# Kernel optimization log

Hardware: AMD Instinct MI355X
Metric: run time of the kernel (lower is better)

## Reference

```python
import math
import jax, jax.numpy as jnp
import numpy as np

B, S, IN_DIM = 8, 1024, 3
D, H, FF, L, OUT = 512, 8, 2048, 4, 6
DH = D // H


def layernorm(x, g, b, eps=1e-5):
    mu = jnp.mean(x, axis=-1, keepdims=True)
    var = jnp.mean((x - mu) ** 2, axis=-1, keepdims=True)
    return (x - mu) * jax.lax.rsqrt(var + eps) * g + b


def positional_encoding(seq_len, d):
    pos = jnp.arange(seq_len, dtype=jnp.float32)[:, None]
    div = jnp.exp(jnp.arange(0, d, 2, dtype=jnp.float32) * (-math.log(10000.0) / d))
    pe = jnp.zeros((seq_len, d), dtype=jnp.float32)
    pe = pe.at[:, 0::2].set(jnp.sin(pos * div))
    pe = pe.at[:, 1::2].set(jnp.cos(pos * div))
    return pe  # [S, D]


def setup_inputs() -> dict:
    key = jax.random.key(0)
    ks = jax.random.split(key, 16)
    s = 0.02
    inp = {
        'x': jax.random.normal(ks[0], (B, S, IN_DIM), dtype=jnp.float32),
        'Wproj': jax.random.normal(ks[1], (IN_DIM, D), dtype=jnp.float32) * s,
        'bproj': jnp.zeros((D,), jnp.float32),
        'gp': jnp.ones((D,), jnp.float32), 'bp': jnp.zeros((D,), jnp.float32),
        'Wq': jax.random.normal(ks[2], (L, D, D), dtype=jnp.float32) * s,
        'Wk': jax.random.normal(ks[3], (L, D, D), dtype=jnp.float32) * s,
        'Wv': jax.random.normal(ks[4], (L, D, D), dtype=jnp.float32) * s,
        'Wo': jax.random.normal(ks[5], (L, D, D), dtype=jnp.float32) * s,
        'g1': jnp.ones((L, D), jnp.float32), 'b1': jnp.zeros((L, D), jnp.float32),
        'W1': jax.random.normal(ks[6], (L, D, FF), dtype=jnp.float32) * s,
        'W2': jax.random.normal(ks[7], (L, FF, D), dtype=jnp.float32) * s,
        'g2': jnp.ones((L, D), jnp.float32), 'b2': jnp.zeros((L, D), jnp.float32),
        'gf': jnp.ones((D,), jnp.float32), 'bf': jnp.zeros((D,), jnp.float32),
        'Wout': jax.random.normal(ks[8], (D, OUT), dtype=jnp.float32) * s,
        'bout': jnp.zeros((OUT,), jnp.float32),
    }
    return inp


def reference(x, Wproj, bproj, gp, bp, Wq, Wk, Wv, Wo, g1, b1,
              W1, W2, g2, b2, gf, bf, Wout, bout):
    # padding mask: True where all features are zero
    mask = jnp.sum(jnp.abs(x), axis=-1) == 0  # [B, S]
    h = x @ Wproj + bproj                     # [B, S, D]
    h = h + positional_encoding(h.shape[1], D)[None]
    h = layernorm(h, gp, bp)
    scale = 1.0 / math.sqrt(DH)
    for l in range(L):
        q = (h @ Wq[l]).reshape(B, S, H, DH)
        k = (h @ Wk[l]).reshape(B, S, H, DH)
        v = (h @ Wv[l]).reshape(B, S, H, DH)
        scores = jnp.einsum('bqhd,bkhd->bhqk', q, k) * scale  # [B,H,S,S]
        scores = jnp.where(mask[:, None, None, :], -jnp.inf, scores)
        attn = jax.nn.softmax(scores, axis=-1)
        o = jnp.einsum('bhqk,bkhd->bqhd', attn, v).reshape(B, S, D) @ Wo[l]
        h = layernorm(h + o, g1[l], b1[l])
        ff = jax.nn.silu(h @ W1[l]) @ W2[l]
        h = layernorm(h + ff, g2[l], b2[l])
    h = layernorm(h, gf, bf)
    not_pad = (~mask).astype(h.dtype)                      # [B, S]
    pooled = jnp.sum(h * not_pad[..., None], axis=1) / (
        jnp.sum(not_pad, axis=1, keepdims=True) + 1e-8)    # [B, D]
    return pooled @ Wout + bout                            # [B, OUT]
```

## Files before the change

### kernel.cpp

```cpp
#include <hip/hip_runtime.h>
#include <math.h>
#include <stdint.h>

namespace {

constexpr int Bc = 8, Sc = 1024, Dc = 512, Hc = 8, FFc = 2048, Lc = 4, OUTc = 6;
constexpr int QS = 1536;

typedef __attribute__((ext_vector_type(8))) short  bf16x8;
typedef __attribute__((ext_vector_type(4))) float  f32x4;

__device__ __forceinline__ void ld4(float d[4], const float* s) {
    float4 t = *(const float4*)s;
    d[0] = t.x; d[1] = t.y; d[2] = t.z; d[3] = t.w;
}
__device__ __forceinline__ float bf2f(unsigned short u) {
    union { uint32_t i; float f; } c; c.i = ((uint32_t)u) << 16; return c.f;
}
__device__ __forceinline__ unsigned short f2bf(float f) {
    union { float f; uint32_t i; } c; c.f = f;
    uint32_t r = c.i + 0x7FFF + ((c.i >> 16) & 1);
    return (unsigned short)(r >> 16);
}

#define GLDS16(gp, lp) __builtin_amdgcn_global_load_lds(                      \
    (const __attribute__((address_space(1))) uint32_t*)(gp),                  \
    (__attribute__((address_space(3))) uint32_t*)(lp), 16, 0, 0)

__global__ __launch_bounds__(256) void castAll(
    const float* __restrict__ Wq, const float* __restrict__ Wk,
    const float* __restrict__ Wv, const float* __restrict__ Wo,
    const float* __restrict__ W1, const float* __restrict__ W2,
    unsigned short* __restrict__ qkvT, unsigned short* __restrict__ WoT,
    unsigned short* __restrict__ W1T, unsigned short* __restrict__ W2T)
{
    const int t = blockIdx.x;
    const float* in; unsigned short* out; int K, N, k0, n0;
    if (t < 1024) {
        const int mat = t >> 6, l = mat >> 2, w = mat & 3;
        K = 512; N = 512;
        k0 = ((t >> 3) & 7) << 6; n0 = (t & 7) << 6;
        const float* ws4[4] = {Wq, Wk, Wv, Wo};
        in = ws4[w] + (size_t)l * 512 * 512;
        out = (w < 3) ? qkvT + (size_t)l * QS * 512 + (size_t)w * 512 * 512
                      : WoT + (size_t)l * 512 * 512;
    } else if (t < 2048) {
        const int u = t - 1024, l = u >> 8;
        K = 512; N = 2048;
        k0 = ((u >> 5) & 7) << 6; n0 = (u & 31) << 6;
        in = W1 + (size_t)l * 512 * 2048;
        out = W1T + (size_t)l * 2048 * 512;
    } else {
        const int u = t - 2048, l = u >> 8;
        K = 2048; N = 512;
        k0 = ((u >> 3) & 31) << 6; n0 = (u & 7) << 6;
        in = W2 + (size_t)l * 2048 * 512;
        out = W2T + (size_t)l * 512 * 2048;
    }
    __shared__ float tbuf[64][65];
    const int c = threadIdx.x & 63, r4 = threadIdx.x >> 6;
    #pragma unroll
    for (int it = 0; it < 16; ++it) {
        const int r = (it << 2) + r4;
        tbuf[r][c] = in[(size_t)(k0 + r) * N + n0 + c];
    }
    __syncthreads();
    #pragma unroll
    for (int it = 0; it < 16; ++it) {
        const int r = (it << 2) + r4;
        out[(size_t)(n0 + r) * K + k0 + c] = f2bf(tbuf[c][r]);
    }
}

__global__ __launch_bounds__(256) void proj_pe_ln(
    const float* __restrict__ x, const float* __restrict__ Wproj,
    const float* __restrict__ bproj, const float* __restrict__ gp,
    const float* __restrict__ bp, float* __restrict__ h,
    unsigned short* __restrict__ hbf, float* __restrict__ notpad,
    float* __restrict__ maskadd)
{
    const int wave = threadIdx.x >> 6, lane = threadIdx.x & 63;
    const int tok = (blockIdx.x << 2) + wave;
    const int s = tok & (Sc - 1);
    const float x0 = x[tok * 3 + 0], x1 = x[tok * 3 + 1], x2 = x[tok * 3 + 2];
    if (lane == 0) {
        const bool pad = (fabsf(x0) + fabsf(x1) + fabsf(x2) == 0.0f);
        notpad[tok]  = pad ? 0.0f : 1.0f;
        maskadd[tok] = pad ? -1e30f : 0.0f;
    }
    const float c = -logf(10000.0f) / (float)Dc;
    float v[8];
    float sum = 0.f, sumsq = 0.f;
    #pragma unroll
    for (int g = 0; g < 2; ++g) {
        const int dbase = (g << 8) + (lane << 2);
        #pragma unroll
        for (int j = 0; j < 4; ++j) {
            const int d = dbase + j;
            float val = fmaf(x0, Wproj[d],
                        fmaf(x1, Wproj[Dc + d],
                        fmaf(x2, Wproj[2 * Dc + d], bproj[d])));
            const float arg = (float)s * expf((float)(d & ~1) * c);
            val += (d & 1) ? cosf(arg) : sinf(arg);
            v[(g << 2) + j] = val;
            sum += val; sumsq += val * val;
        }
    }
    #pragma unroll
    for (int m = 1; m < 64; m <<= 1) {
        sum   += __shfl_xor(sum, m, 64);
        sumsq += __shfl_xor(sumsq, m, 64);
    }
    const float mu = sum * (1.0f / Dc);
    const float var = sumsq * (1.0f / Dc) - mu * mu;
    const float rstd = rsqrtf(var + 1e-5f);
    #pragma unroll
    for (int g = 0; g < 2; ++g) {
        const int dbase = (g << 8) + (lane << 2);
        float gg[4], bb[4];
        ld4(gg, gp + dbase); ld4(bb, bp + dbase);
        float4 r;
        r.x = (v[(g<<2)+0] - mu) * rstd * gg[0] + bb[0];
        r.y = (v[(g<<2)+1] - mu) * rstd * gg[1] + bb[1];
        r.z = (v[(g<<2)+2] - mu) * rstd * gg[2] + bb[2];
        r.w = (v[(g<<2)+3] - mu) * rstd * gg[3] + bb[3];
        *(float4*)(h + (size_t)tok * Dc + dbase) = r;
        ushort4 rb;
        rb.x = f2bf(r.x); rb.y = f2bf(r.y); rb.z = f2bf(r.z); rb.w = f2bf(r.w);
        *(ushort4*)(hbf + (size_t)tok * Dc + dbase) = rb;
    }
}

__global__ __launch_bounds__(256) void add_ln(
    const float* __restrict__ hin, const unsigned short* __restrict__ delta,
    const float* __restrict__ g, const float* __restrict__ b,
    float* __restrict__ hout, unsigned short* __restrict__ hbf)
{
    const int wave = threadIdx.x >> 6, lane = threadIdx.x & 63;
    const int tok = (blockIdx.x << 2) + wave;
    const float* hp = hin + (size_t)tok * Dc;
    float v[8];
    float sum = 0.f, sumsq = 0.f;
    #pragma unroll
    for (int gI = 0; gI < 2; ++gI) {
        const int dbase = (gI << 8) + (lane << 2);
        float a[4];
        ld4(a, hp + dbase);
        if (delta) {
            ushort4 d4 = *(const ushort4*)(delta + (size_t)tok * Dc + dbase);
            a[0] += bf2f(d4.x); a[1] += bf2f(d4.y);
            a[2] += bf2f(d4.z); a[3] += bf2f(d4.w);
        }
        #pragma unroll
        for (int j = 0; j < 4; ++j) {
            v[(gI << 2) + j] = a[j];
            sum += a[j]; sumsq += a[j] * a[j];
        }
    }
    #pragma unroll
    for (int m = 1; m < 64; m <<= 1) {
        sum   += __shfl_xor(sum, m, 64);
        sumsq += __shfl_xor(sumsq, m, 64);
    }
    const float mu = sum * (1.0f / Dc);
    const float var = sumsq * (1.0f / Dc) - mu * mu;
    const float rstd = rsqrtf(var + 1e-5f);
    #pragma unroll
    for (int gI = 0; gI < 2; ++gI) {
        const int dbase = (gI << 8) + (lane << 2);
        float gg[4], bb[4];
        ld4(gg, g + dbase); ld4(bb, b + dbase);
        float4 r;
        r.x = (v[(gI<<2)+0] - mu) * rstd * gg[0] + bb[0];
        r.y = (v[(gI<<2)+1] - mu) * rstd * gg[1] + bb[1];
        r.z = (v[(gI<<2)+2] - mu) * rstd * gg[2] + bb[2];
        r.w = (v[(gI<<2)+3] - mu) * rstd * gg[3] + bb[3];
        *(float4*)(hout + (size_t)tok * Dc + dbase) = r;
        if (hbf) {
            ushort4 rb;
            rb.x = f2bf(r.x); rb.y = f2bf(r.y); rb.z = f2bf(r.z); rb.w = f2bf(r.w);
            *(ushort4*)(hbf + (size_t)tok * Dc + dbase) = rb;
        }
    }
}

template<int EPI, int NT>
__global__ __launch_bounds__(256) void gemm_bf16(
    const unsigned short* __restrict__ A, const unsigned short* __restrict__ Bt,
    void* __restrict__ Cv, void* __restrict__ Cv2, int M, int N, int K)
{
    constexpr int JN = NT / 32;
    constexpr int ABsz = 128 * 64 + NT * 64;
    constexpr int TRst = 136;
    constexpr int SMsz = (EPI == 3 && 128 * TRst > ABsz) ? 128 * TRst : ABsz;
    __shared__ unsigned short smem[SMsz];
    unsigned short* As = smem;
    unsigned short* Bs = smem + 128 * 64;
    const int tid = threadIdx.x;
    const int wave = tid >> 6, lane = tid & 63;
    const int m0 = blockIdx.y << 7;
    const int n0 = blockIdx.x * NT;
    const int wm = (wave >> 1) << 6;
    const int wn = (wave & 1) * (NT / 2);
    const int l15 = lane & 15;
    const int lg  = lane >> 4;
    const int grow  = lane >> 3;
    const int gcolk = ((lane & 7) ^ grow) << 3;

    f32x4 acc[4][JN] = {};

    for (int k0 = 0; k0 < K; k0 += 64) {
        __syncthreads();
        #pragma unroll
        for (int t = 0; t < 4; ++t) {
            const int rb = (t << 5) + (wave << 3);
            GLDS16(A + (size_t)(m0 + rb + grow) * K + k0 + gcolk, &As[rb * 64]);
        }
        #pragma unroll
        for (int t = 0; t < NT / 32; ++t) {
            const int rb = (t << 5) + (wave << 3);
            GLDS16(Bt + (size_t)(n0 + rb + grow) * K + k0 + gcolk, &Bs[rb * 64]);
        }
        __syncthreads();
        #pragma unroll
        for (int h = 0; h < 2; ++h) {
            const int sw = (((h << 2) + lg) ^ (l15 & 7)) << 3;
            bf16x8 af[4], bfr[JN];
            #pragma unroll
            for (int i = 0; i < 4; ++i)
                af[i] = *(const bf16x8*)&As[(wm + (i << 4) + l15) * 64 + sw];
            #pragma unroll
            for (int j = 0; j < JN; ++j)
                bfr[j] = *(const bf16x8*)&Bs[(wn + (j << 4) + l15) * 64 + sw];
            #pragma unroll
            for (int i = 0; i < 4; ++i)
                #pragma unroll
                for (int j = 0; j < JN; ++j)
                    acc[i][j] = __builtin_amdgcn_mfma_f32_16x16x32_bf16(
                        af[i], bfr[j], acc[i][j], 0, 0, 0);
        }
    }

    if constexpr (EPI == 3) {
        if (n0 >= 1024) {
            __syncthreads();
            unsigned short* Tr = smem;
            #pragma unroll
            for (int i = 0; i < 4; ++i)
                #pragma unroll
                for (int j = 0; j < JN; ++j)
                    #pragma unroll
                    for (int r = 0; r < 4; ++r)
                        Tr[(wn + (j << 4) + l15) * TRst + wm + (i << 4) + (lg << 2) + r]
                            = f2bf(acc[i][j][r]);
            __syncthreads();
            const int bb = m0 >> 10, s0 = m0 & 1023;
            #pragma unroll
            for (int it = 0; it < 8; ++it) {
                const int idx = (it << 8) + tid;
                const int ln = idx >> 4, lmc = (idx & 15) << 3;
                const int gcol = n0 - 1024 + ln;
                const int head = gcol >> 6, dh = gcol & 63;
                *(bf16x8*)((unsigned short*)Cv2 +
                    (size_t)((((bb << 3) + head) << 6) + dh) * 1024 + s0 + lmc) =
                    *(const bf16x8*)&Tr[ln * TRst + lmc];
            }
            return;
        }
    }

    const int crow0 = m0 + wm + (lg << 2);
    const int ccol0 = n0 + wn + l15;
    #pragma unroll
    for (int i = 0; i < 4; ++i)
        #pragma unroll
        for (int j = 0; j < JN; ++j)
            #pragma unroll
            for (int r = 0; r < 4; ++r) {
                const int row = crow0 + (i << 4) + r;
                const int col = ccol0 + (j << 4);
                float v = acc[i][j][r];
                if (EPI == 3) {
                    if (n0 < 512) v *= 0.125f;
                    ((unsigned short*)Cv)[(size_t)row * 1024 + col] = f2bf(v);
                } else {
                    if (EPI == 1) v = v / (1.0f + expf(-v));
                    ((unsigned short*)Cv)[(size_t)row * N + col] = f2bf(v);
                }
            }
}

__global__ __launch_bounds__(256, 2) void attn_mfma(
    const unsigned short* __restrict__ qk,
    const unsigned short* __restrict__ vT,
    const float* __restrict__ maskadd,
    unsigned short* __restrict__ o)
{
    constexpr int PST = 124;
    __shared__ unsigned short Ks[2][128][32];
    __shared__ unsigned short Vs[4][64][32];
    __shared__ unsigned short Ps[4][32][PST];
    __shared__ float Madd[128];
    const int tid = threadIdx.x;
    const int wave = tid >> 6, lane = tid & 63;
    const int b  = blockIdx.x & 7;
    const int hh = (blockIdx.x >> 3) & 7;
    const int qt = blockIdx.x >> 6;
    const int q0 = qt << 7;
    const int l15 = lane & 15, lg = lane >> 4;
    const int srow = lane >> 2;
    const int scol = (lane & 3) << 3;

    #pragma unroll
    for (int t = 0; t < 2; ++t)
        #pragma unroll
        for (int p = 0; p < 2; ++p)
            GLDS16(qk + (size_t)((b << 10) + q0 + (t << 6) + (wave << 4) + srow) * 1024
                      + (hh << 6) + (p << 5) + scol,
                   &Ks[p][(t << 6) + (wave << 4)][0]);
    __syncthreads();
    bf16x8 qf[2][2];
    #pragma unroll
    for (int s = 0; s < 2; ++s)
        #pragma unroll
        for (int p = 0; p < 2; ++p)
            qf[s][p] = *(const bf16x8*)&Ks[p][(s << 6) + (wave << 4) + l15][lg << 3];

    f32x4 oacc[2][4] = {};
    float l_part[2][4] = {};

    for (int kt = 0; kt < 8; ++kt) {
        const int k0 = kt << 7;
        __syncthreads();
        #pragma unroll
        for (int t = 0; t < 2; ++t)
            #pragma unroll
            for (int p = 0; p < 2; ++p)
                GLDS16(qk + (size_t)((b << 10) + k0 + (t << 6) + (wave << 4) + srow) * 1024
                          + 512 + (hh << 6) + (p << 5) + scol,
                       &Ks[p][(t << 6) + (wave << 4)][0]);
        #pragma unroll
        for (int kp = 0; kp < 4; ++kp)
            GLDS16(vT + (size_t)((((b << 3) + hh) << 6) + (wave << 4) + srow) * 1024
                      + k0 + (kp << 5) + scol,
                   &Vs[kp][wave << 4][0]);
        if (tid < 128) Madd[tid] = maskadd[(b << 10) + k0 + tid];
        __syncthreads();

        f32x4 sacc[2][8] = {};
        #pragma unroll
        for (int j = 0; j < 8; ++j) {
            const bf16x8 kf0 = *(const bf16x8*)&Ks[0][(j << 4) + l15][lg << 3];
            const bf16x8 kf1 = *(const bf16x8*)&Ks[1][(j << 4) + l15][lg << 3];
            #pragma unroll
            for (int s = 0; s < 2; ++s) {
                sacc[s][j] = __builtin_amdgcn_mfma_f32_16x16x32_bf16(qf[s][0], kf0, sacc[s][j], 0, 0, 0);
                sacc[s][j] = __builtin_amdgcn_mfma_f32_16x16x32_bf16(qf[s][1], kf1, sacc[s][j], 0, 0, 0);
            }
        }

        #pragma unroll
        for (int s = 0; s < 2; ++s)
            #pragma unroll
            for (int j = 0; j < 8; ++j) {
                const float ma = Madd[(j << 4) + l15];
                #pragma unroll
                for (int r = 0; r < 4; ++r) {
                    const float p = __expf(sacc[s][j][r] + ma);
                    l_part[s][r] += p;
                    Ps[wave][(s << 4) + (lg << 2) + r][(j << 4) + l15] = f2bf(p);
                }
            }
        __asm__ volatile("s_waitcnt lgkmcnt(0)" ::: "memory");

        #pragma unroll
        for (int kp = 0; kp < 4; ++kp) {
            bf16x8 vf[4];
            #pragma unroll
            for (int j = 0; j < 4; ++j)
                vf[j] = *(const bf16x8*)&Vs[kp][(j << 4) + l15][lg << 3];
            #pragma unroll
            for (int s = 0; s < 2; ++s) {
                const bf16x8 pa = *(const bf16x8*)&Ps[wave][(s << 4) + l15][(kp << 5) + (lg << 3)];
                #pragma unroll
                for (int j = 0; j < 4; ++j)
                    oacc[s][j] = __builtin_amdgcn_mfma_f32_16x16x32_bf16(pa, vf[j], oacc[s][j], 0, 0, 0);
            }
        }
    }

    #pragma unroll
    for (int s = 0; s < 2; ++s)
        #pragma unroll
        for (int r = 0; r < 4; ++r) {
            float l = l_part[s][r];
            #pragma unroll
            for (int m = 1; m < 16; m <<= 1) l += __shfl_xor(l, m, 64);
            l_part[s][r] = 1.0f / l;
        }
    #pragma unroll
    for (int s = 0; s < 2; ++s) {
        const int tokr = (b << 10) + q0 + (s << 6) + (wave << 4) + (lg << 2);
        #pragma unroll
        for (int j = 0; j < 4; ++j)
            #pragma unroll
            for (int r = 0; r < 4; ++r)
                o[(size_t)(tokr + r) * 512 + (hh << 6) + (j << 4) + l15] =
                    f2bf(oacc[s][j][r] * l_part[s][r]);
    }
}

__global__ __launch_bounds__(256) void pool_kernel(
    const float* __restrict__ h, const float* __restrict__ notpad,
    float* __restrict__ pooled, float* __restrict__ counts)
{
    const int b = blockIdx.y;
    const int s0 = blockIdx.x << 5;
    const int t = threadIdx.x;
    float a0 = 0.f, a1 = 0.f;
    for (int ss = 0; ss < 32; ++ss) {
        const float w = notpad[(b << 10) + s0 + ss];
        const float* hp = h + (size_t)((b << 10) + s0 + ss) * Dc;
        a0 = fmaf(w, hp[t], a0);
        a1 = fmaf(w, hp[t + 256], a1);
    }
    atomicAdd(&pooled[b * Dc + t], a0);
    atomicAdd(&pooled[b * Dc + t + 256], a1);
    if (t < 32) {
        float w = notpad[(b << 10) + s0 + t];
        #pragma unroll
        for (int m = 1; m < 32; m <<= 1) w += __shfl_xor(w, m, 64);
        if (t == 0) atomicAdd(&counts[b], w);
    }
}

__global__ void out_kernel(
    const float* __restrict__ pooled, const float* __restrict__ counts,
    const float* __restrict__ Wout, const float* __restrict__ bout,
    float* __restrict__ out)
{
    const int bo = blockIdx.x;
    const int b = bo / OUTc, oc = bo % OUTc;
    const int lane = threadIdx.x;
    float acc = 0.f;
    for (int d = lane; d < Dc; d += 64)
        acc = fmaf(pooled[b * Dc + d], Wout[(size_t)d * OUTc + oc], acc);
    #pragma unroll
    for (int m = 1; m < 64; m <<= 1) acc += __shfl_xor(acc, m, 64);
    if (lane == 0) out[b * OUTc + oc] = acc / (counts[b] + 1e-8f) + bout[oc];
}

}

extern "C" void kernel_launch(void* const* d_in, const int* in_sizes, int n_in,
                              void* d_out, int out_size, void* d_ws, size_t ws_size,
                              hipStream_t stream)
{
    (void)in_sizes; (void)n_in; (void)out_size; (void)ws_size;
    const float* x     = (const float*)d_in[0];
    const float* Wproj = (const float*)d_in[1];
    const float* bproj = (const float*)d_in[2];
    const float* gp    = (const float*)d_in[3];
    const float* bp    = (const float*)d_in[4];
    const float* Wq    = (const float*)d_in[5];
    const float* Wk    = (const float*)d_in[6];
    const float* Wv    = (const float*)d_in[7];
    const float* Wo    = (const float*)d_in[8];
    const float* g1    = (const float*)d_in[9];
    const float* b1    = (const float*)d_in[10];
    const float* W1    = (const float*)d_in[11];
    const float* W2    = (const float*)d_in[12];
    const float* g2    = (const float*)d_in[13];
    const float* b2    = (const float*)d_in[14];
    const float* gf    = (const float*)d_in[15];
    const float* bf    = (const float*)d_in[16];
    const float* Wout  = (const float*)d_in[17];
    const float* bout  = (const float*)d_in[18];
    float* out = (float*)d_out;

    const size_t MiB = 1u << 20;
    char* base = (char*)d_ws;
    float*          h       = (float*)(base);
    unsigned short* h_bf    = (unsigned short*)(base + 16 * MiB);
    unsigned short* qk_act  = (unsigned short*)(base + 24 * MiB);
    unsigned short* vT      = (unsigned short*)(base + 40 * MiB);
    unsigned short* ob_bf   = (unsigned short*)(base + 48 * MiB);
    unsigned short* bufB_bf = (unsigned short*)(base + 56 * MiB);
    unsigned short* ffa_bf  = (unsigned short*)(base + 24 * MiB);
    unsigned short* qkvT    = (unsigned short*)(base + 72 * MiB);
    unsigned short* WoT     = (unsigned short*)(base + 78 * MiB);
    unsigned short* W1T     = (unsigned short*)(base + 80 * MiB);
    unsigned short* W2T     = (unsigned short*)(base + 88 * MiB);
    float*          notpad  = (float*)(base + 96 * MiB);
    float*          maskadd = notpad + 8192;
    float*          pooled  = maskadd + 8192;
    float*          counts  = pooled + Bc * Dc;

    const int M = Bc * Sc;

    castAll<<<3072, 256, 0, stream>>>(Wq, Wk, Wv, Wo, W1, W2, qkvT, WoT, W1T, W2T);
    proj_pe_ln<<<M / 4, 256, 0, stream>>>(x, Wproj, bproj, gp, bp, h, h_bf, notpad, maskadd);

    for (int l = 0; l < Lc; ++l) {
        gemm_bf16<3, 128><<<dim3(QS / 128, M / 128), 256, 0, stream>>>(
            h_bf, qkvT + (size_t)l * QS * 512, qk_act, vT, M, QS, 512);
        attn_mfma<<<Bc * Hc * (Sc / 128), 256, 0, stream>>>(qk_act, vT, maskadd, ob_bf);
        gemm_bf16<2, 64><<<dim3(512 / 64, M / 128), 256, 0, stream>>>(
            ob_bf, WoT + (size_t)l * 512 * 512, bufB_bf, nullptr, M, 512, 512);
        add_ln<<<M / 4, 256, 0, stream>>>(h, bufB_bf, g1 + (size_t)l * Dc, b1 + (size_t)l * Dc, h, h_bf);
        gemm_bf16<1, 128><<<dim3(FFc / 128, M / 128), 256, 0, stream>>>(
            h_bf, W1T + (size_t)l * FFc * 512, ffa_bf, nullptr, M, FFc, 512);
        gemm_bf16<2, 64><<<dim3(512 / 64, M / 128), 256, 0, stream>>>(
            ffa_bf, W2T + (size_t)l * 512 * FFc, bufB_bf, nullptr, M, 512, FFc);
        add_ln<<<M / 4, 256, 0, stream>>>(h, bufB_bf, g2 + (size_t)l * Dc, b2 + (size_t)l * Dc, h, h_bf);
    }
    add_ln<<<M / 4, 256, 0, stream>>>(h, nullptr, gf, bf, h, nullptr);

    hipMemsetAsync(pooled, 0, (size_t)(Bc * Dc + Bc) * sizeof(float), stream);
    pool_kernel<<<dim3(Sc / 32, Bc), 256, 0, stream>>>(h, notpad, pooled, counts);
    out_kernel<<<Bc * OUTc, 64, 0, stream>>>(pooled, counts, Wout, bout, out);
}
```

Before: 816.2 us.

## Keep residual in bf16, fuse final LN into pooling, coalesce GEMM epilogue

Removes the fp32 residual buffer so layernorm kernels read and write only bf16, halving residual traffic. The final layernorm is fused into the pooling kernel, and GEMM epilogues stage results through shared memory for vectorized coalesced stores. The attention kernel folds log2(e) into the Q scale to use exp2, uses cheaper bf16 rounding, and restructures P staging to halve shared memory. These changes trade residual precision for bandwidth and reduce kernel count.

```diff
diff --git a/kernel.cpp b/kernel.cpp
--- a/kernel.cpp
+++ b/kernel.cpp
@@ -16,11 +16,18 @@
 }
 __device__ __forceinline__ float bf2f(unsigned short u) {
     union { uint32_t i; float f; } c; c.i = ((uint32_t)u) << 16; return c.f;
+}
+__device__ __forceinline__ float bf2f_s(short u) {
+    union { uint32_t i; float f; } c; c.i = ((uint32_t)(unsigned short)u) << 16; return c.f;
 }
 __device__ __forceinline__ unsigned short f2bf(float f) {
     union { float f; uint32_t i; } c; c.f = f;
     uint32_t r = c.i + 0x7FFF + ((c.i >> 16) & 1);
     return (unsigned short)(r >> 16);
+}
+__device__ __forceinline__ unsigned short f2bf_fast(float f) {
+    union { float f; uint32_t i; } c; c.f = f;
+    return (unsigned short)((c.i + 0x8000u) >> 16);
 }
 
 #define GLDS16(gp, lp) __builtin_amdgcn_global_load_lds(                      \
@@ -75,9 +82,8 @@
 __global__ __launch_bounds__(256) void proj_pe_ln(
     const float* __restrict__ x, const float* __restrict__ Wproj,
     const float* __restrict__ bproj, const float* __restrict__ gp,
-    const float* __restrict__ bp, float* __restrict__ h,
-    unsigned short* __restrict__ hbf, float* __restrict__ notpad,
-    float* __restrict__ maskadd)
+    const float* __restrict__ bp, unsigned short* __restrict__ hbf,
+    float* __restrict__ notpad, float* __restrict__ maskadd)
 {
     const int wave = threadIdx.x >> 6, lane = threadIdx.x & 63;
     const int tok = (blockIdx.x << 2) + wave;
@@ -91,20 +97,17 @@
     const float c = -logf(10000.0f) / (float)Dc;
     float v[8];
     float sum = 0.f, sumsq = 0.f;
-    #pragma unroll
-    for (int g = 0; g < 2; ++g) {
-        const int dbase = (g << 8) + (lane << 2);
-        #pragma unroll
-        for (int j = 0; j < 4; ++j) {
-            const int d = dbase + j;
-            float val = fmaf(x0, Wproj[d],
-                        fmaf(x1, Wproj[Dc + d],
-                        fmaf(x2, Wproj[2 * Dc + d], bproj[d])));
-            const float arg = (float)s * expf((float)(d & ~1) * c);
-            val += (d & 1) ? cosf(arg) : sinf(arg);
-            v[(g << 2) + j] = val;
-            sum += val; sumsq += val * val;
-        }
+    const int d0 = lane << 3;
+    #pragma unroll
+    for (int j = 0; j < 8; ++j) {
+        const int d = d0 + j;
+        float val = fmaf(x0, Wproj[d],
+                    fmaf(x1, Wproj[Dc + d],
+                    fmaf(x2, Wproj[2 * Dc + d], bproj[d])));
+        const float arg = (float)s * expf((float)(d & ~1) * c);
+        val += (d & 1) ? cosf(arg) : sinf(arg);
+        v[j] = val;
+        sum += val; sumsq += val * val;
     }
     #pragma unroll
     for (int m = 1; m < 64; m <<= 1) {
@@ -112,50 +115,34 @@
         sumsq += __shfl_xor(sumsq, m, 64);
     }
     const float mu = sum * (1.0f / Dc);
-    const float var = sumsq * (1.0f / Dc) - mu * mu;
-    const float rstd = rsqrtf(var + 1e-5f);
-    #pragma unroll
-    for (int g = 0; g < 2; ++g) {
-        const int dbase = (g << 8) + (lane << 2);
-        float gg[4], bb[4];
-        ld4(gg, gp + dbase); ld4(bb, bp + dbase);
-        float4 r;
-        r.x = (v[(g<<2)+0] - mu) * rstd * gg[0] + bb[0];
-        r.y = (v[(g<<2)+1] - mu) * rstd * gg[1] + bb[1];
-        r.z = (v[(g<<2)+2] - mu) * rstd * gg[2] + bb[2];
-        r.w = (v[(g<<2)+3] - mu) * rstd * gg[3] + bb[3];
-        *(float4*)(h + (size_t)tok * Dc + dbase) = r;
-        ushort4 rb;
-        rb.x = f2bf(r.x); rb.y = f2bf(r.y); rb.z = f2bf(r.z); rb.w = f2bf(r.w);
-        *(ushort4*)(hbf + (size_t)tok * Dc + dbase) = rb;
-    }
+    const float rstd = rsqrtf(sumsq * (1.0f / Dc) - mu * mu + 1e-5f);
+    float gg[8], bb[8];
+    ld4(gg, gp + d0); ld4(gg + 4, gp + d0 + 4);
+    ld4(bb, bp + d0); ld4(bb + 4, bp + d0 + 4);
+    bf16x8 rb;
+    #pragma unroll
+    for (int j = 0; j < 8; ++j)
+        rb[j] = (short)f2bf((v[j] - mu) * rstd * gg[j] + bb[j]);
+    *(bf16x8*)(hbf + (size_t)tok * Dc + d0) = rb;
 }
 
 __global__ __launch_bounds__(256) void add_ln(
-    const float* __restrict__ hin, const unsigned short* __restrict__ delta,
+    const unsigned short* __restrict__ hin, const unsigned short* __restrict__ delta,
     const float* __restrict__ g, const float* __restrict__ b,
-    float* __restrict__ hout, unsigned short* __restrict__ hbf)
+    unsigned short* __restrict__ hout)
 {
     const int wave = threadIdx.x >> 6, lane = threadIdx.x & 63;
     const int tok = (blockIdx.x << 2) + wave;
-    const float* hp = hin + (size_t)tok * Dc;
+    const int d0 = lane << 3;
+    const size_t base = (size_t)tok * Dc + d0;
+    const bf16x8 hv = *(const bf16x8*)(hin + base);
+    const bf16x8 dv = *(const bf16x8*)(delta + base);
     float v[8];
     float sum = 0.f, sumsq = 0.f;
     #pragma unroll
-    for (int gI = 0; gI < 2; ++gI) {
-        const int dbase = (gI << 8) + (lane << 2);
-        float a[4];
-        ld4(a, hp + dbase);
-        if (delta) {
-            ushort4 d4 = *(const ushort4*)(delta + (size_t)tok * Dc + dbase);
-            a[0] += bf2f(d4.x); a[1] += bf2f(d4.y);
-            a[2] += bf2f(d4.z); a[3] += bf2f(d4.w);
-        }
-        #pragma unroll
-        for (int j = 0; j < 4; ++j) {
-            v[(gI << 2) + j] = a[j];
-            sum += a[j]; sumsq += a[j] * a[j];
-        }
+    for (int j = 0; j < 8; ++j) {
+        v[j] = bf2f_s(hv[j]) + bf2f_s(dv[j]);
+        sum += v[j]; sumsq += v[j] * v[j];
     }
     #pragma unroll
     for (int m = 1; m < 64; m <<= 1) {
@@ -163,25 +150,15 @@
         sumsq += __shfl_xor(sumsq, m, 64);
     }
     const float mu = sum * (1.0f / Dc);
-    const float var = sumsq * (1.0f / Dc) - mu * mu;
-    const float rstd = rsqrtf(var + 1e-5f);
-    #pragma unroll
-    for (int gI = 0; gI < 2; ++gI) {
-        const int dbase = (gI << 8) + (lane << 2);
-        float gg[4], bb[4];
-        ld4(gg, g + dbase); ld4(bb, b + dbase);
-        float4 r;
-        r.x = (v[(gI<<2)+0] - mu) * rstd * gg[0] + bb[0];
-        r.y = (v[(gI<<2)+1] - mu) * rstd * gg[1] + bb[1];
-        r.z = (v[(gI<<2)+2] - mu) * rstd * gg[2] + bb[2];
-        r.w = (v[(gI<<2)+3] - mu) * rstd * gg[3] + bb[3];
-        *(float4*)(hout + (size_t)tok * Dc + dbase) = r;
-        if (hbf) {
-            ushort4 rb;
-            rb.x = f2bf(r.x); rb.y = f2bf(r.y); rb.z = f2bf(r.z); rb.w = f2bf(r.w);
-            *(ushort4*)(hbf + (size_t)tok * Dc + dbase) = rb;
-        }
-    }
+    const float rstd = rsqrtf(sumsq * (1.0f / Dc) - mu * mu + 1e-5f);
+    float gg[8], bb[8];
+    ld4(gg, g + d0); ld4(gg + 4, g + d0 + 4);
+    ld4(bb, b + d0); ld4(bb + 4, b + d0 + 4);
+    bf16x8 rb;
+    #pragma unroll
+    for (int j = 0; j < 8; ++j)
+        rb[j] = (short)f2bf((v[j] - mu) * rstd * gg[j] + bb[j]);
+    *(bf16x8*)(hout + base) = rb;
 }
 
 template<int EPI, int NT>
@@ -190,9 +167,10 @@
     void* __restrict__ Cv, void* __restrict__ Cv2, int M, int N, int K)
 {
     constexpr int JN = NT / 32;
+    constexpr int TR = NT + 12;
     constexpr int ABsz = 128 * 64 + NT * 64;
-    constexpr int TRst = 136;
-    constexpr int SMsz = (EPI == 3 && 128 * TRst > ABsz) ? 128 * TRst : ABsz;
+    constexpr int TrSz = 128 * TR;
+    constexpr int SMsz = (ABsz > TrSz) ? ABsz : TrSz;
     __shared__ unsigned short smem[SMsz];
     unsigned short* As = smem;
     unsigned short* Bs = smem + 128 * 64;
@@ -241,17 +219,18 @@
         }
     }
 
+    __syncthreads();
+    unsigned short* Tr = smem;
+
     if constexpr (EPI == 3) {
         if (n0 >= 1024) {
-            __syncthreads();
-            unsigned short* Tr = smem;
             #pragma unroll
             for (int i = 0; i < 4; ++i)
                 #pragma unroll
                 for (int j = 0; j < JN; ++j)
                     #pragma unroll
                     for (int r = 0; r < 4; ++r)
-                        Tr[(wn + (j << 4) + l15) * TRst + wm + (i << 4) + (lg << 2) + r]
+                        Tr[(wn + (j << 4) + l15) * TR + wm + (i << 4) + (lg << 2) + r]
                             = f2bf(acc[i][j][r]);
             __syncthreads();
             const int bb = m0 >> 10, s0 = m0 & 1023;
@@ -263,43 +242,46 @@
                 const int head = gcol >> 6, dh = gcol & 63;
                 *(bf16x8*)((unsigned short*)Cv2 +
                     (size_t)((((bb << 3) + head) << 6) + dh) * 1024 + s0 + lmc) =
-                    *(const bf16x8*)&Tr[ln * TRst + lmc];
+                    *(const bf16x8*)&Tr[ln * TR + lmc];
             }
             return;
         }
     }
 
-    const int crow0 = m0 + wm + (lg << 2);
-    const int ccol0 = n0 + wn + l15;
+    const float qsc = 0.125f * 1.44269504f;
     #pragma unroll
     for (int i = 0; i < 4; ++i)
         #pragma unroll
         for (int j = 0; j < JN; ++j)
             #pragma unroll
             for (int r = 0; r < 4; ++r) {
-                const int row = crow0 + (i << 4) + r;
-                const int col = ccol0 + (j << 4);
                 float v = acc[i][j][r];
-                if (EPI == 3) {
-                    if (n0 < 512) v *= 0.125f;
-                    ((unsigned short*)Cv)[(size_t)row * 1024 + col] = f2bf(v);
-                } else {
-                    if (EPI == 1) v = v / (1.0f + expf(-v));
-                    ((unsigned short*)Cv)[(size_t)row * N + col] = f2bf(v);
-                }
+                if (EPI == 1) v = v / (1.0f + expf(-v));
+                if (EPI == 3 && n0 < 512) v *= qsc;
+                Tr[(wm + (i << 4) + (lg << 2) + r) * TR + wn + (j << 4) + l15] = f2bf(v);
             }
-}
-
-__global__ __launch_bounds__(256, 2) void attn_mfma(
+    __syncthreads();
+    const int ldo = (EPI == 3) ? 1024 : N;
+    constexpr int CPR = NT / 8;
+    #pragma unroll
+    for (int it = 0; it < (128 * CPR) / 256; ++it) {
+        const int idx = (it << 8) + tid;
+        const int row = idx / CPR, cc = (idx % CPR) << 3;
+        *(bf16x8*)((unsigned short*)Cv + (size_t)(m0 + row) * ldo + n0 + cc) =
+            *(const bf16x8*)&Tr[row * TR + cc];
+    }
+}
+
+__global__ __launch_bounds__(256) void attn_mfma(
     const unsigned short* __restrict__ qk,
     const unsigned short* __restrict__ vT,
     const float* __restrict__ maskadd,
     unsigned short* __restrict__ o)
 {
-    constexpr int PST = 124;
+    constexpr int PST = 132;
     __shared__ unsigned short Ks[2][128][32];
     __shared__ unsigned short Vs[4][64][32];
-    __shared__ unsigned short Ps[4][32][PST];
+    __shared__ unsigned short Ps[4][16][PST];
     __shared__ float Madd[128];
     const int tid = threadIdx.x;
     const int wave = tid >> 6, lane = tid & 63;
@@ -359,33 +341,36 @@
             }
         }
 
-        #pragma unroll
-        for (int s = 0; s < 2; ++s)
-            #pragma unroll
-            for (int j = 0; j < 8; ++j) {
-                const float ma = Madd[(j << 4) + l15];
+        bf16x8 vf[4][4];
+        #pragma unroll
+        for (int kp = 0; kp < 4; ++kp)
+            #pragma unroll
+            for (int j = 0; j < 4; ++j)
+                vf[kp][j] = *(const bf16x8*)&Vs[kp][(j << 4) + l15][lg << 3];
+
+        float ma[8];
+        #pragma unroll
+        for (int j = 0; j < 8; ++j) ma[j] = Madd[(j << 4) + l15];
+
+        #pragma unroll
+        for (int s = 0; s < 2; ++s) {
+            #pragma unroll
+            for (int j = 0; j < 8; ++j)
                 #pragma unroll
                 for (int r = 0; r < 4; ++r) {
-                    const float p = __expf(sacc[s][j][r] + ma);
+                    const float p = exp2f(sacc[s][j][r] + ma[j]);
                     l_part[s][r] += p;
-                    Ps[wave][(s << 4) + (lg << 2) + r][(j << 4) + l15] = f2bf(p);
+                    Ps[wave][(lg << 2) + r][(j << 4) + l15] = f2bf_fast(p);
                 }
-            }
-        __asm__ volatile("s_waitcnt lgkmcnt(0)" ::: "memory");
-
-        #pragma unroll
-        for (int kp = 0; kp < 4; ++kp) {
-            bf16x8 vf[4];
-            #pragma unroll
-            for (int j = 0; j < 4; ++j)
-                vf[j] = *(const bf16x8*)&Vs[kp][(j << 4) + l15][lg << 3];
-            #pragma unroll
-            for (int s = 0; s < 2; ++s) {
-                const bf16x8 pa = *(const bf16x8*)&Ps[wave][(s << 4) + l15][(kp << 5) + (lg << 3)];
+            __asm__ volatile("s_waitcnt lgkmcnt(0)" ::: "memory");
+            #pragma unroll
+            for (int kp = 0; kp < 4; ++kp) {
+                const bf16x8 pa = *(const bf16x8*)&Ps[wave][l15][(kp << 5) + (lg << 3)];
                 #pragma unroll
                 for (int j = 0; j < 4; ++j)
-                    oacc[s][j] = __builtin_amdgcn_mfma_f32_16x16x32_bf16(pa, vf[j], oacc[s][j], 0, 0, 0);
+                    oacc[s][j] = __builtin_amdgcn_mfma_f32_16x16x32_bf16(pa, vf[kp][j], oacc[s][j], 0, 0, 0);
             }
+            __asm__ volatile("s_waitcnt lgkmcnt(0)" ::: "memory");
         }
     }
 
@@ -410,27 +395,51 @@
     }
 }
 
-__global__ __launch_bounds__(256) void pool_kernel(
-    const float* __restrict__ h, const float* __restrict__ notpad,
+__global__ __launch_bounds__(256) void pool_ln(
+    const unsigned short* __restrict__ hbf, const float* __restrict__ notpad,
+    const float* __restrict__ gf, const float* __restrict__ bfp,
     float* __restrict__ pooled, float* __restrict__ counts)
 {
-    const int b = blockIdx.y;
-    const int s0 = blockIdx.x << 5;
-    const int t = threadIdx.x;
-    float a0 = 0.f, a1 = 0.f;
-    for (int ss = 0; ss < 32; ++ss) {
-        const float w = notpad[(b << 10) + s0 + ss];
-        const float* hp = h + (size_t)((b << 10) + s0 + ss) * Dc;
-        a0 = fmaf(w, hp[t], a0);
-        a1 = fmaf(w, hp[t + 256], a1);
-    }
-    atomicAdd(&pooled[b * Dc + t], a0);
-    atomicAdd(&pooled[b * Dc + t + 256], a1);
-    if (t < 32) {
-        float w = notpad[(b << 10) + s0 + t];
+    __shared__ float sh[512];
+    const int b = blockIdx.y, s0 = blockIdx.x << 5;
+    const int wave = threadIdx.x >> 6, lane = threadIdx.x & 63;
+    const int d0 = lane << 3;
+    float gg[8], bb[8];
+    ld4(gg, gf + d0); ld4(gg + 4, gf + d0 + 4);
+    ld4(bb, bfp + d0); ld4(bb + 4, bfp + d0 + 4);
+    float accv[8] = {};
+    for (int t = 0; t < 8; ++t) {
+        const int tok = (b << 10) + s0 + (wave << 3) + t;
+        const float w = notpad[tok];
+        const bf16x8 hv = *(const bf16x8*)(hbf + (size_t)tok * Dc + d0);
+        float v[8], sum = 0.f, sumsq = 0.f;
+        #pragma unroll
+        for (int j = 0; j < 8; ++j) {
+            v[j] = bf2f_s(hv[j]); sum += v[j]; sumsq += v[j] * v[j];
+        }
+        #pragma unroll
+        for (int m = 1; m < 64; m <<= 1) {
+            sum   += __shfl_xor(sum, m, 64);
+            sumsq += __shfl_xor(sumsq, m, 64);
+        }
+        const float mu = sum * (1.0f / Dc);
+        const float rstd = rsqrtf(sumsq * (1.0f / Dc) - mu * mu + 1e-5f);
+        #pragma unroll
+        for (int j = 0; j < 8; ++j)
+            accv[j] = fmaf(w, (v[j] - mu) * rstd * gg[j] + bb[j], accv[j]);
+    }
+    sh[threadIdx.x] = 0.f; sh[threadIdx.x + 256] = 0.f;
+    __syncthreads();
+    #pragma unroll
+    for (int j = 0; j < 8; ++j) atomicAdd(&sh[d0 + j], accv[j]);
+    __syncthreads();
+    atomicAdd(&pooled[b * Dc + threadIdx.x], sh[threadIdx.x]);
+    atomicAdd(&pooled[b * Dc + 256 + threadIdx.x], sh[threadIdx.x + 256]);
+    if (threadIdx.x < 32) {
+        float w = notpad[(b << 10) + s0 + threadIdx.x];
         #pragma unroll
         for (int m = 1; m < 32; m <<= 1) w += __shfl_xor(w, m, 64);
-        if (t == 0) atomicAdd(&counts[b], w);
+        if (threadIdx.x == 0) atomicAdd(&counts[b], w);
     }
 }
 
@@ -480,8 +489,7 @@
 
     const size_t MiB = 1u << 20;
     char* base = (char*)d_ws;
-    float*          h       = (float*)(base);
-    unsigned short* h_bf    = (unsigned short*)(base + 16 * MiB);
+    unsigned short* h_bf    = (unsigned short*)(base);
     unsigned short* qk_act  = (unsigned short*)(base + 24 * MiB);
     unsigned short* vT      = (unsigned short*)(base + 40 * MiB);
     unsigned short* ob_bf   = (unsigned short*)(base + 48 * MiB);
@@ -499,7 +507,7 @@
     const int M = Bc * Sc;
 
     castAll<<<3072, 256, 0, stream>>>(Wq, Wk, Wv, Wo, W1, W2, qkvT, WoT, W1T, W2T);
-    proj_pe_ln<<<M / 4, 256, 0, stream>>>(x, Wproj, bproj, gp, bp, h, h_bf, notpad, maskadd);
+    proj_pe_ln<<<M / 4, 256, 0, stream>>>(x, Wproj, bproj, gp, bp, h_bf, notpad, maskadd);
 
     for (int l = 0; l < Lc; ++l) {
         gemm_bf16<3, 128><<<dim3(QS / 128, M / 128), 256, 0, stream>>>(
@@ -507,16 +515,15 @@
         attn_mfma<<<Bc * Hc * (Sc / 128), 256, 0, stream>>>(qk_act, vT, maskadd, ob_bf);
         gemm_bf16<2, 64><<<dim3(512 / 64, M / 128), 256, 0, stream>>>(
             ob_bf, WoT + (size_t)l * 512 * 512, bufB_bf, nullptr, M, 512, 512);
-        add_ln<<<M / 4, 256, 0, stream>>>(h, bufB_bf, g1 + (size_t)l * Dc, b1 + (size_t)l * Dc, h, h_bf);
+        add_ln<<<M / 4, 256, 0, stream>>>(h_bf, bufB_bf, g1 + (size_t)l * Dc, b1 + (size_t)l * Dc, h_bf);
         gemm_bf16<1, 128><<<dim3(FFc / 128, M / 128), 256, 0, stream>>>(
             h_bf, W1T + (size_t)l * FFc * 512, ffa_bf, nullptr, M, FFc, 512);
         gemm_bf16<2, 64><<<dim3(512 / 64, M / 128), 256, 0, stream>>>(
             ffa_bf, W2T + (size_t)l * 512 * FFc, bufB_bf, nullptr, M, 512, FFc);
-        add_ln<<<M / 4, 256, 0, stream>>>(h, bufB_bf, g2 + (size_t)l * Dc, b2 + (size_t)l * Dc, h, h_bf);
-    }
-    add_ln<<<M / 4, 256, 0, stream>>>(h, nullptr, gf, bf, h, nullptr);
+        add_ln<<<M / 4, 256, 0, stream>>>(h_bf, bufB_bf, g2 + (size_t)l * Dc, b2 + (size_t)l * Dc, h_bf);
+    }
 
     hipMemsetAsync(pooled, 0, (size_t)(Bc * Dc + Bc) * sizeof(float), stream);
-    pool_kernel<<<dim3(Sc / 32, Bc), 256, 0, stream>>>(h, notpad, pooled, counts);
+    pool_ln<<<dim3(Sc / 32, Bc), 256, 0, stream>>>(h_bf, notpad, gf, bf, pooled, counts);
     out_kernel<<<Bc * OUTc, 64, 0, stream>>>(pooled, counts, Wout, bout, out);
 }
```

Result: slower. 862.4 us (+5.7%).
